# Performance work log

Measured on AMD Instinct MI355X. Metric: run time of the kernel, lower is better.

Reference implementation:

```python
import jax, jax.numpy as jnp
import numpy as np

Z, P, CIN, COUT, E, HID = 4, 512, 32, 32, 65536, 128

def setup_inputs() -> dict:
    key = jax.random.key(0)
    ks = jax.random.split(key, 8)
    return {
        "features": jax.random.normal(ks[0], (Z, P, CIN), dtype=jnp.float32),
        "edge_vec": jax.random.normal(ks[1], (E, 3), dtype=jnp.float32),
        "W1": jax.random.normal(ks[2], (4, HID), dtype=jnp.float32) * 0.5,
        "b1": jax.random.normal(ks[3], (HID,), dtype=jnp.float32) * 0.1,
        "W2": jax.random.normal(ks[4], (HID, COUT * CIN), dtype=jnp.float32) * (1.0 / np.sqrt(HID)),
        "edge_batch": jax.random.randint(ks[5], (E,), 0, Z),
        "edge_a": jax.random.randint(ks[6], (E,), 0, P),
        "edge_b": jax.random.randint(ks[7], (E,), 0, P),
        "n_norm": 1,
    }

def reference(features, edge_vec, W1, b1, W2, edge_batch, edge_a, edge_b, n_norm):
    Zb, Pn, Cin = features.shape
    # zero near-degenerate radii (matches radius[norm < 1e-10] = 0)
    r = jnp.linalg.norm(edge_vec, axis=-1, keepdims=True)  # [E,1]
    vec = jnp.where(r < 1e-10, jnp.zeros_like(edge_vec), edge_vec)
    rn = jnp.where(r < 1e-10, jnp.zeros_like(r), r)
    # per-edge kernel: MLP(vec, |vec|) -> [E, c_out, c_in]
    x = jnp.concatenate([vec, rn], axis=-1)               # [E,4]
    h = jax.nn.relu(x @ W1 + b1)                          # [E,HID]
    Cout = W2.shape[1] // Cin
    k = (h @ W2).reshape(-1, Cout, Cin)                   # [E,co,ci]
    # gather neighbor features, per-edge matvec, scatter-add to centers
    f_b = features[edge_batch, edge_b]                    # [E,ci]
    msg = jnp.einsum('eij,ej->ei', k, f_b)                # [E,co]
    seg = edge_batch * Pn + edge_a
    out = jax.ops.segment_sum(msg, seg, num_segments=Zb * Pn)
    out = out.reshape(Zb, Pn, Cout)
    return out / jnp.sqrt(jnp.asarray(n_norm, dtype=features.dtype))
```

## Files before the change

kernel.cpp:

```cpp
#include <hip/hip_runtime.h>
#include <hip/hip_bf16.h>

#define ZBATCH 4
#define PN     512
#define CINC   32
#define COUTC  32
#define EN     65536
#define HIDN   128
#define NNODE  (ZBATCH*PN)
#define JD     (HIDN*COUTC)
#define CAP    128

__global__ void bin_k(const int* __restrict__ eb, const int* __restrict__ ea,
                      const int* __restrict__ ebn,
                      int* __restrict__ cnt_src, int* __restrict__ cnt_dst,
                      int* __restrict__ order_src, int* __restrict__ order_dst) {
  const int e = blockIdx.x * 256 + threadIdx.x;
  const int zb = eb[e];
  const int ns = zb * PN + ebn[e];
  const int nd = zb * PN + ea[e];
  const int p = atomicAdd(&cnt_src[ns], 1);
  if (p < CAP) order_src[ns * CAP + p] = e;
  const int q = atomicAdd(&cnt_dst[nd], 1);
  if (q < CAP) order_dst[nd * CAP + q] = e;
}

__global__ __launch_bounds__(256) void pass1_k(const float* __restrict__ F,
                                               const float* __restrict__ W2,
                                               __hip_bfloat16* __restrict__ Wf) {
  const int t = threadIdx.x;
  const int j = blockIdx.x * 256 + t;
  const int n0 = blockIdx.y * 16;
  const int h = j >> 5, co = j & 31;
  const float4* w4 = (const float4*)(W2 + h * (COUTC * CINC) + co * CINC);
  float w[32];
#pragma unroll
  for (int q = 0; q < 8; ++q) {
    const float4 x = w4[q];
    w[4 * q] = x.x; w[4 * q + 1] = x.y; w[4 * q + 2] = x.z; w[4 * q + 3] = x.w;
  }
  for (int n = 0; n < 16; ++n) {
    const float* fr = F + (size_t)(n0 + n) * CINC;
    float acc = 0.f;
#pragma unroll
    for (int ci = 0; ci < 32; ++ci) acc = fmaf(fr[ci], w[ci], acc);
    Wf[(size_t)(n0 + n) * JD + j] = __float2bfloat16(acc);
  }
}

__global__ __launch_bounds__(256) void pass2m_k(
    const float* __restrict__ evec, const float* __restrict__ W1,
    const float* __restrict__ b1, const __hip_bfloat16* __restrict__ Wf,
    const int* __restrict__ cnt_src, const int* __restrict__ order_src,
    const int* __restrict__ nn, float* __restrict__ msg) {
  const int n = blockIdx.x;
  const int t = threadIdx.x;
  const int lane = t & 63;
  const int w = t >> 6;
  const int co = lane & 31;
  const int hh = lane >> 5;

  __shared__ float w1s[4][HIDN];
  __shared__ float b1s[HIDN];
  __shared__ __align__(16) float Hbuf[4][8][HIDN];

  const int count0 = cnt_src[n];
  const int count = count0 < CAP ? count0 : CAP;
  if (count == 0) return;

  for (int i = t; i < 4 * HIDN; i += 256) w1s[i >> 7][i & 127] = W1[i];
  for (int i = t; i < HIDN; i += 256) b1s[i] = b1[i];

  float wf[64];
  {
    const __hip_bfloat16* wp = Wf + (size_t)n * JD + hh * 64 * COUTC + co;
#pragma unroll
    for (int j = 0; j < 64; ++j) wf[j] = __bfloat162float(wp[(size_t)j * COUTC]);
  }
  const float scale = rsqrtf((float)nn[0]);
  __syncthreads();

  const int h0 = lane << 1;
  const int* ord = order_src + (size_t)n * CAP;
  for (int base = w * 8; base < count; base += 32) {
    const int nb = (count - base < 8) ? (count - base) : 8;
    for (int i = 0; i < nb; ++i) {
      const int e = ord[base + i];
      const float x0 = evec[3 * e], x1 = evec[3 * e + 1], x2 = evec[3 * e + 2];
      const float r = sqrtf(x0 * x0 + x1 * x1 + x2 * x2);
      const bool bad = (r < 1e-10f);
      const float y0 = bad ? 0.f : x0, y1 = bad ? 0.f : x1;
      const float y2 = bad ? 0.f : x2, y3 = bad ? 0.f : r;
      float a0 = b1s[h0]     + y0 * w1s[0][h0]     + y1 * w1s[1][h0]
                             + y2 * w1s[2][h0]     + y3 * w1s[3][h0];
      float a1 = b1s[h0 + 1] + y0 * w1s[0][h0 + 1] + y1 * w1s[1][h0 + 1]
                             + y2 * w1s[2][h0 + 1] + y3 * w1s[3][h0 + 1];
      float2 hv;
      hv.x = fmaxf(a0, 0.f);
      hv.y = fmaxf(a1, 0.f);
      *(float2*)(&Hbuf[w][i][h0]) = hv;
    }
    __builtin_amdgcn_wave_barrier();
    for (int i = 0; i < nb; ++i) {
      const int e = ord[base + i];
      const float* hp = &Hbuf[w][i][hh * 64];
      float acc = 0.f;
#pragma unroll
      for (int k = 0; k < 16; ++k) {
        const float4 h4 = *(const float4*)(hp + 4 * k);
        acc = fmaf(h4.x, wf[4 * k],     acc);
        acc = fmaf(h4.y, wf[4 * k + 1], acc);
        acc = fmaf(h4.z, wf[4 * k + 2], acc);
        acc = fmaf(h4.w, wf[4 * k + 3], acc);
      }
      acc += __shfl_xor(acc, 32);
      if (hh == 0) msg[(size_t)e * COUTC + co] = acc * scale;
    }
    __builtin_amdgcn_wave_barrier();
  }
}

__global__ __launch_bounds__(64) void reduce_k(const float* __restrict__ msg,
                                               const int* __restrict__ cnt_dst,
                                               const int* __restrict__ order_dst,
                                               float* __restrict__ out) {
  const int n = blockIdx.x;
  const int t = threadIdx.x;
  const int co = t & 31;
  const int hh = t >> 5;
  __shared__ int idxs[CAP];
  const int c0 = cnt_dst[n];
  const int count = c0 < CAP ? c0 : CAP;
  for (int i = t; i < count; i += 64) idxs[i] = order_dst[(size_t)n * CAP + i];
  __syncthreads();
  float acc = 0.f;
#pragma unroll 4
  for (int i = hh; i < count; i += 2) acc += msg[(size_t)idxs[i] * COUTC + co];
  acc += __shfl_xor(acc, 32);
  if (t < 32) out[(size_t)n * COUTC + co] = acc;
}

extern "C" void kernel_launch(void* const* d_in, const int* in_sizes, int n_in,
                              void* d_out, int out_size, void* d_ws, size_t ws_size,
                              hipStream_t stream) {
  const float* features   = (const float*)d_in[0];
  const float* edge_vec   = (const float*)d_in[1];
  const float* W1         = (const float*)d_in[2];
  const float* b1         = (const float*)d_in[3];
  const float* W2         = (const float*)d_in[4];
  const int*   edge_batch = (const int*)d_in[5];
  const int*   edge_a     = (const int*)d_in[6];
  const int*   edge_b     = (const int*)d_in[7];
  const int*   n_norm     = (const int*)d_in[8];
  float* out = (float*)d_out;

  char* ws = (char*)d_ws;
  __hip_bfloat16* Wf = (__hip_bfloat16*)ws;
  float* msg = (float*)(ws + (size_t)NNODE * JD * 2);
  int* ints = (int*)(ws + (size_t)NNODE * JD * 2 + (size_t)EN * COUTC * 4);
  int* cnt_src   = ints;
  int* cnt_dst   = ints + NNODE;
  int* order_src = ints + 2 * NNODE;
  int* order_dst = ints + 2 * NNODE + NNODE * CAP;
  const size_t need = (size_t)NNODE * JD * 2 + (size_t)EN * COUTC * 4
                    + (size_t)(2 * NNODE + 2 * NNODE * CAP) * 4;
  if (ws_size < need) return;

  hipMemsetAsync(cnt_src, 0, 2 * NNODE * 4, stream);
  bin_k<<<EN / 256, 256, 0, stream>>>(edge_batch, edge_a, edge_b,
                                      cnt_src, cnt_dst, order_src, order_dst);
  pass1_k<<<dim3(16, 128), 256, 0, stream>>>(features, W2, Wf);
  pass2m_k<<<NNODE, 256, 0, stream>>>(edge_vec, W1, b1, Wf, cnt_src, order_src,
                                      n_norm, msg);
  reduce_k<<<NNODE, 64, 0, stream>>>(msg, cnt_dst, order_dst, out);
}
```

Before: 148.3 us.

## Fuse all stages into one persistent cooperative kernel with grid syncs

Replaces the memset and four separate kernel launches (binning, feature-weight precompute, per-node MLP messages, destination reduction) with one cooperative kernel that loops over the work with grid-stride loops and separates the stages with grid.sync. The goal is to remove launch and inter-kernel gaps. In exchange, the grid is capped at 512 persistent blocks, so each block takes several nodes in sequence. Grid-wide barriers add their own cost, and the reduction stage no longer stages indices in shared memory.

Measured after the change: 391.1 us. 2.64x slower.

```diff
diff --git a/kernel.cpp b/kernel.cpp
--- a/kernel.cpp
+++ b/kernel.cpp
@@ -1,5 +1,7 @@
 #include <hip/hip_runtime.h>
 #include <hip/hip_bf16.h>
+#include <hip/hip_cooperative_groups.h>
+namespace cg = cooperative_groups;
 
 #define ZBATCH 4
 #define PN     512
@@ -11,133 +13,127 @@
 #define JD     (HIDN*COUTC)
 #define CAP    128
 
-__global__ void bin_k(const int* __restrict__ eb, const int* __restrict__ ea,
-                      const int* __restrict__ ebn,
-                      int* __restrict__ cnt_src, int* __restrict__ cnt_dst,
-                      int* __restrict__ order_src, int* __restrict__ order_dst) {
-  const int e = blockIdx.x * 256 + threadIdx.x;
-  const int zb = eb[e];
-  const int ns = zb * PN + ebn[e];
-  const int nd = zb * PN + ea[e];
-  const int p = atomicAdd(&cnt_src[ns], 1);
-  if (p < CAP) order_src[ns * CAP + p] = e;
-  const int q = atomicAdd(&cnt_dst[nd], 1);
-  if (q < CAP) order_dst[nd * CAP + q] = e;
-}
+__global__ __launch_bounds__(256) void mega_k(
+    const float* __restrict__ F, const float* __restrict__ evec,
+    const float* __restrict__ W1, const float* __restrict__ b1,
+    const float* __restrict__ W2, const int* __restrict__ eb,
+    const int* __restrict__ ea, const int* __restrict__ ebn,
+    const int* __restrict__ nn, float* __restrict__ out,
+    __hip_bfloat16* __restrict__ Wf, float* __restrict__ msg,
+    int* __restrict__ ints) {
+  cg::grid_group grid = cg::this_grid();
+  int* cnt_src   = ints;
+  int* cnt_dst   = ints + NNODE;
+  int* order_src = ints + 2 * NNODE;
+  int* order_dst = order_src + NNODE * CAP;
 
-__global__ __launch_bounds__(256) void pass1_k(const float* __restrict__ F,
-                                               const float* __restrict__ W2,
-                                               __hip_bfloat16* __restrict__ Wf) {
-  const int t = threadIdx.x;
-  const int j = blockIdx.x * 256 + t;
-  const int n0 = blockIdx.y * 16;
-  const int h = j >> 5, co = j & 31;
-  const float4* w4 = (const float4*)(W2 + h * (COUTC * CINC) + co * CINC);
-  float w[32];
-#pragma unroll
-  for (int q = 0; q < 8; ++q) {
-    const float4 x = w4[q];
-    w[4 * q] = x.x; w[4 * q + 1] = x.y; w[4 * q + 2] = x.z; w[4 * q + 3] = x.w;
-  }
-  for (int n = 0; n < 16; ++n) {
-    const float* fr = F + (size_t)(n0 + n) * CINC;
-    float acc = 0.f;
-#pragma unroll
-    for (int ci = 0; ci < 32; ++ci) acc = fmaf(fr[ci], w[ci], acc);
-    Wf[(size_t)(n0 + n) * JD + j] = __float2bfloat16(acc);
-  }
-}
-
-__global__ __launch_bounds__(256) void pass2m_k(
-    const float* __restrict__ evec, const float* __restrict__ W1,
-    const float* __restrict__ b1, const __hip_bfloat16* __restrict__ Wf,
-    const int* __restrict__ cnt_src, const int* __restrict__ order_src,
-    const int* __restrict__ nn, float* __restrict__ msg) {
-  const int n = blockIdx.x;
-  const int t = threadIdx.x;
-  const int lane = t & 63;
-  const int w = t >> 6;
-  const int co = lane & 31;
-  const int hh = lane >> 5;
+  const int t = threadIdx.x, b = blockIdx.x, nblk = gridDim.x;
+  const int gtid = b * 256 + t, gstr = nblk * 256;
 
   __shared__ float w1s[4][HIDN];
   __shared__ float b1s[HIDN];
   __shared__ __align__(16) float Hbuf[4][8][HIDN];
 
-  const int count0 = cnt_src[n];
-  const int count = count0 < CAP ? count0 : CAP;
-  if (count == 0) return;
+  for (int i = gtid; i < 2 * NNODE; i += gstr) cnt_src[i] = 0;
+  grid.sync();
 
+  for (int e = gtid; e < EN; e += gstr) {
+    const int zb = eb[e];
+    const int ns = zb * PN + ebn[e];
+    const int nd = zb * PN + ea[e];
+    const int p = atomicAdd(&cnt_src[ns], 1);
+    if (p < CAP) order_src[ns * CAP + p] = e;
+    const int q = atomicAdd(&cnt_dst[nd], 1);
+    if (q < CAP) order_dst[nd * CAP + q] = e;
+  }
   for (int i = t; i < 4 * HIDN; i += 256) w1s[i >> 7][i & 127] = W1[i];
   for (int i = t; i < HIDN; i += 256) b1s[i] = b1[i];
+  grid.sync();
 
-  float wf[64];
-  {
-    const __hip_bfloat16* wp = Wf + (size_t)n * JD + hh * 64 * COUTC + co;
+  for (int u = b; u < 2048; u += nblk) {
+    const int j = (u & 15) * 256 + t;
+    const int n0 = (u >> 4) * 16;
+    const int h = j >> 5, co = j & 31;
+    const float4* w4 = (const float4*)(W2 + h * (COUTC * CINC) + co * CINC);
+    float w[32];
 #pragma unroll
-    for (int j = 0; j < 64; ++j) wf[j] = __bfloat162float(wp[(size_t)j * COUTC]);
-  }
-  const float scale = rsqrtf((float)nn[0]);
-  __syncthreads();
-
-  const int h0 = lane << 1;
-  const int* ord = order_src + (size_t)n * CAP;
-  for (int base = w * 8; base < count; base += 32) {
-    const int nb = (count - base < 8) ? (count - base) : 8;
-    for (int i = 0; i < nb; ++i) {
-      const int e = ord[base + i];
-      const float x0 = evec[3 * e], x1 = evec[3 * e + 1], x2 = evec[3 * e + 2];
-      const float r = sqrtf(x0 * x0 + x1 * x1 + x2 * x2);
-      const bool bad = (r < 1e-10f);
-      const float y0 = bad ? 0.f : x0, y1 = bad ? 0.f : x1;
-      const float y2 = bad ? 0.f : x2, y3 = bad ? 0.f : r;
-      float a0 = b1s[h0]     + y0 * w1s[0][h0]     + y1 * w1s[1][h0]
-                             + y2 * w1s[2][h0]     + y3 * w1s[3][h0];
-      float a1 = b1s[h0 + 1] + y0 * w1s[0][h0 + 1] + y1 * w1s[1][h0 + 1]
-                             + y2 * w1s[2][h0 + 1] + y3 * w1s[3][h0 + 1];
-      float2 hv;
-      hv.x = fmaxf(a0, 0.f);
-      hv.y = fmaxf(a1, 0.f);
-      *(float2*)(&Hbuf[w][i][h0]) = hv;
+    for (int q = 0; q < 8; ++q) {
+      const float4 x = w4[q];
+      w[4 * q] = x.x; w[4 * q + 1] = x.y; w[4 * q + 2] = x.z; w[4 * q + 3] = x.w;
     }
-    __builtin_amdgcn_wave_barrier();
-    for (int i = 0; i < nb; ++i) {
-      const int e = ord[base + i];
-      const float* hp = &Hbuf[w][i][hh * 64];
+    for (int n = 0; n < 16; ++n) {
+      const float* fr = F + (size_t)(n0 + n) * CINC;
       float acc = 0.f;
 #pragma unroll
-      for (int k = 0; k < 16; ++k) {
-        const float4 h4 = *(const float4*)(hp + 4 * k);
-        acc = fmaf(h4.x, wf[4 * k],     acc);
-        acc = fmaf(h4.y, wf[4 * k + 1], acc);
-        acc = fmaf(h4.z, wf[4 * k + 2], acc);
-        acc = fmaf(h4.w, wf[4 * k + 3], acc);
+      for (int ci = 0; ci < 32; ++ci) acc = fmaf(fr[ci], w[ci], acc);
+      Wf[(size_t)(n0 + n) * JD + j] = __float2bfloat16(acc);
+    }
+  }
+  grid.sync();
+
+  const int lane = t & 63, w = t >> 6;
+  const int co = lane & 31, hh = lane >> 5;
+  const float scale = rsqrtf((float)nn[0]);
+  const int h0 = lane << 1;
+  for (int n = b; n < NNODE; n += nblk) {
+    const int c0 = cnt_src[n];
+    const int count = c0 < CAP ? c0 : CAP;
+    if (count == 0) continue;
+    float wf[64];
+    {
+      const __hip_bfloat16* wp = Wf + (size_t)n * JD + hh * 64 * COUTC + co;
+#pragma unroll
+      for (int j = 0; j < 64; ++j) wf[j] = __bfloat162float(wp[(size_t)j * COUTC]);
+    }
+    const int* ord = order_src + (size_t)n * CAP;
+    for (int base = w * 8; base < count; base += 32) {
+      const int nb = (count - base < 8) ? (count - base) : 8;
+      for (int i = 0; i < nb; ++i) {
+        const int e = ord[base + i];
+        const float x0 = evec[3 * e], x1 = evec[3 * e + 1], x2 = evec[3 * e + 2];
+        const float r = sqrtf(x0 * x0 + x1 * x1 + x2 * x2);
+        const bool bad = (r < 1e-10f);
+        const float y0 = bad ? 0.f : x0, y1 = bad ? 0.f : x1;
+        const float y2 = bad ? 0.f : x2, y3 = bad ? 0.f : r;
+        float a0 = b1s[h0]     + y0 * w1s[0][h0]     + y1 * w1s[1][h0]
+                               + y2 * w1s[2][h0]     + y3 * w1s[3][h0];
+        float a1 = b1s[h0 + 1] + y0 * w1s[0][h0 + 1] + y1 * w1s[1][h0 + 1]
+                               + y2 * w1s[2][h0 + 1] + y3 * w1s[3][h0 + 1];
+        float2 hv;
+        hv.x = fmaxf(a0, 0.f);
+        hv.y = fmaxf(a1, 0.f);
+        *(float2*)(&Hbuf[w][i][h0]) = hv;
       }
-      acc += __shfl_xor(acc, 32);
-      if (hh == 0) msg[(size_t)e * COUTC + co] = acc * scale;
+      __builtin_amdgcn_wave_barrier();
+      for (int i = 0; i < nb; ++i) {
+        const int e = ord[base + i];
+        const float* hp = &Hbuf[w][i][hh * 64];
+        float acc = 0.f;
+#pragma unroll
+        for (int k = 0; k < 16; ++k) {
+          const float4 h4 = *(const float4*)(hp + 4 * k);
+          acc = fmaf(h4.x, wf[4 * k],     acc);
+          acc = fmaf(h4.y, wf[4 * k + 1], acc);
+          acc = fmaf(h4.z, wf[4 * k + 2], acc);
+          acc = fmaf(h4.w, wf[4 * k + 3], acc);
+        }
+        acc += __shfl_xor(acc, 32);
+        if (hh == 0) msg[(size_t)e * COUTC + co] = acc * scale;
+      }
+      __builtin_amdgcn_wave_barrier();
     }
-    __builtin_amdgcn_wave_barrier();
   }
-}
+  grid.sync();
 
-__global__ __launch_bounds__(64) void reduce_k(const float* __restrict__ msg,
-                                               const int* __restrict__ cnt_dst,
-                                               const int* __restrict__ order_dst,
-                                               float* __restrict__ out) {
-  const int n = blockIdx.x;
-  const int t = threadIdx.x;
-  const int co = t & 31;
-  const int hh = t >> 5;
-  __shared__ int idxs[CAP];
-  const int c0 = cnt_dst[n];
-  const int count = c0 < CAP ? c0 : CAP;
-  for (int i = t; i < count; i += 64) idxs[i] = order_dst[(size_t)n * CAP + i];
-  __syncthreads();
-  float acc = 0.f;
-#pragma unroll 4
-  for (int i = hh; i < count; i += 2) acc += msg[(size_t)idxs[i] * COUTC + co];
-  acc += __shfl_xor(acc, 32);
-  if (t < 32) out[(size_t)n * COUTC + co] = acc;
+  for (int n = b * 4 + w; n < NNODE; n += nblk * 4) {
+    const int c0 = cnt_dst[n];
+    const int count = c0 < CAP ? c0 : CAP;
+    float acc = 0.f;
+    for (int i = hh; i < count; i += 2)
+      acc += msg[(size_t)order_dst[(size_t)n * CAP + i] * COUTC + co];
+    acc += __shfl_xor(acc, 32);
+    if (hh == 0) out[(size_t)n * COUTC + co] = acc;
+  }
 }
 
 extern "C" void kernel_launch(void* const* d_in, const int* in_sizes, int n_in,
@@ -158,19 +154,22 @@
   __hip_bfloat16* Wf = (__hip_bfloat16*)ws;
   float* msg = (float*)(ws + (size_t)NNODE * JD * 2);
   int* ints = (int*)(ws + (size_t)NNODE * JD * 2 + (size_t)EN * COUTC * 4);
-  int* cnt_src   = ints;
-  int* cnt_dst   = ints + NNODE;
-  int* order_src = ints + 2 * NNODE;
-  int* order_dst = ints + 2 * NNODE + NNODE * CAP;
   const size_t need = (size_t)NNODE * JD * 2 + (size_t)EN * COUTC * 4
                     + (size_t)(2 * NNODE + 2 * NNODE * CAP) * 4;
   if (ws_size < need) return;
 
-  hipMemsetAsync(cnt_src, 0, 2 * NNODE * 4, stream);
-  bin_k<<<EN / 256, 256, 0, stream>>>(edge_batch, edge_a, edge_b,
-                                      cnt_src, cnt_dst, order_src, order_dst);
-  pass1_k<<<dim3(16, 128), 256, 0, stream>>>(features, W2, Wf);
-  pass2m_k<<<NNODE, 256, 0, stream>>>(edge_vec, W1, b1, Wf, cnt_src, order_src,
-                                      n_norm, msg);
-  reduce_k<<<NNODE, 64, 0, stream>>>(msg, cnt_dst, order_dst, out);
+  int nblk = 512;
+  int maxb = 0;
+  if (hipOccupancyMaxActiveBlocksPerMultiprocessor(&maxb, mega_k, 256, 0)
+          == hipSuccess && maxb > 0) {
+    const int cap = maxb * 256;
+    if (cap < nblk) nblk = cap;
+  }
+  void* args[] = {
+    (void*)&features, (void*)&edge_vec, (void*)&W1, (void*)&b1, (void*)&W2,
+    (void*)&edge_batch, (void*)&edge_a, (void*)&edge_b, (void*)&n_norm,
+    (void*)&out, (void*)&Wf, (void*)&msg, (void*)&ints
+  };
+  hipLaunchCooperativeKernel((void*)mega_k, dim3(nblk), dim3(256), args, 0,
+                             stream);
 }
```
